# Optimization experiments

Measured on AMD Instinct MI355X. Metric: run time of the kernel, lower is better.

## Reference

```python
import jax, jax.numpy as jnp
import numpy as np

N_SAMPLES = 8_388_608   # total packed samples (~64 per ray on average)
N_RAYS = 131_072
DT_SCALE = 0.005        # keep per-ray optical depth ~O(1); also tempers global-cumsum fp32 error


def setup_inputs() -> dict:
    key = jax.random.key(0)
    k1, k2, k3, k4, k5 = jax.random.split(key, 5)
    rgb_samples = jax.random.uniform(k1, (N_SAMPLES, 3), dtype=jnp.float32)
    radiance_samples = jax.random.uniform(k2, (N_SAMPLES, 1), dtype=jnp.float32)  # density sigma >= 0
    samples_z = jax.random.uniform(k3, (N_SAMPLES,), dtype=jnp.float32)           # t values in [0,1)
    samples_dt = jax.random.uniform(k4, (N_SAMPLES,), dtype=jnp.float32) * DT_SCALE
    # sorted segment ids == contiguous packed per-ray sample ranges (ragged)
    ray_id = jnp.sort(jax.random.randint(k5, (N_SAMPLES,), 0, N_RAYS, dtype=jnp.int64))
    ray_t_exit = jnp.full((N_RAYS, 1), 2.0, dtype=jnp.float32)  # exit t beyond all z -> positive last dt
    return {
        "rgb_samples": rgb_samples,
        "radiance_samples": radiance_samples,
        "samples_z": samples_z,
        "samples_dt": samples_dt,
        "ray_id": ray_id,
        "ray_t_exit": ray_t_exit,
        "use_ray_t_exit": 1,
    }


def reference(rgb_samples, radiance_samples, samples_z, samples_dt, ray_id, ray_t_exit, use_ray_t_exit):
    N = rgb_samples.shape[0]
    sigma = radiance_samples[:, 0]
    idx = jnp.arange(N)

    # dt of the last sample of each ray is (t_exit - z_last) when use_ray_t_exit
    if use_ray_t_exit:
        last_idx = jax.ops.segment_max(idx, ray_id, num_segments=N_RAYS)
        is_last = idx == last_idx[ray_id]
        dt = jnp.where(is_last, ray_t_exit[ray_id, 0] - samples_z, samples_dt)
    else:
        dt = samples_dt

    sigdt = sigma * dt                      # optical depth per sample
    c = jnp.cumsum(sigdt)                   # global inclusive cumsum
    c_excl = c - sigdt                      # global exclusive cumsum
    # exclusive cumsum restarted per ray: subtract value at each segment's first sample
    # (c_excl is non-decreasing since sigdt >= 0, so segment_min == first element)
    seg_start = jax.ops.segment_min(c_excl, ray_id, num_segments=N_RAYS)
    T = jnp.exp(-(c_excl - seg_start[ray_id]))          # transmittance before each sample
    alpha = 1.0 - jnp.exp(-sigdt)
    w = alpha * T                                        # per-sample compositing weight

    pred_rgb = jax.ops.segment_sum(w[:, None] * rgb_samples, ray_id, num_segments=N_RAYS)   # [R,3]
    pred_depth = jax.ops.segment_sum(w * samples_z, ray_id, num_segments=N_RAYS)[:, None]   # [R,1]
    bg_transmittance = jnp.exp(-jax.ops.segment_sum(sigdt, ray_id, num_segments=N_RAYS))[:, None]  # [R,1]
    weight_per_sample = w[:, None]                                                           # [N,1]
    return pred_rgb, pred_depth, bg_transmittance, weight_per_sample
```

## Files before the change

kernel.cpp:

```cpp
#include <hip/hip_runtime.h>


#define RPW 4

struct F3 { float x, y, z; };

template <int CTRL, int ROW_MASK>
__device__ __forceinline__ float dpp_add(float x) {
    int t = __builtin_amdgcn_update_dpp(0, __float_as_int(x), CTRL, ROW_MASK, 0xf, true);
    return x + __int_as_float(t);
}

__device__ __forceinline__ float wave_incl_scan(float x) {
    x = dpp_add<0x111, 0xf>(x);
    x = dpp_add<0x112, 0xf>(x);
    x = dpp_add<0x114, 0xf>(x);
    x = dpp_add<0x118, 0xf>(x);
    x = dpp_add<0x142, 0xa>(x);
    x = dpp_add<0x143, 0xc>(x);
    return x;
}

__device__ __forceinline__ float readlane_f32(float x, int lane) {
    return __int_as_float(__builtin_amdgcn_readlane(__float_as_int(x), lane));
}

__global__ void compute_starts_kernel(const int* __restrict__ ray_id,
                                      int n_samples, int n_rays,
                                      int* __restrict__ starts) {
    const int t = blockIdx.x * blockDim.x + threadIdx.x;
    const int stride = gridDim.x * blockDim.x;
    if (t == 0) {
        const int first = ray_id[0];
        for (int r = 0; r <= first; ++r) starts[r] = 0;
        const int last = ray_id[n_samples - 1];
        for (int r = last + 1; r <= n_rays; ++r) starts[r] = n_samples;
    }
    for (int g = t; g * 4 < n_samples; g += stride) {
        const int i4 = g * 4;
        const int4 v = *reinterpret_cast<const int4*>(ray_id + i4);
        const int prev = (i4 == 0) ? v.x : ray_id[i4 - 1];
        const int vals[5] = {prev, v.x, v.y, v.z, v.w};
        #pragma unroll
        for (int j = 0; j < 4; ++j) {
            const int p = vals[j], c = vals[j + 1];
            if (c != p) {
                for (int r = p + 1; r <= c; ++r) starts[r] = i4 + j;
            }
        }
    }
}

__device__ __forceinline__ void process_chunk64(
    float sg, float zv, float dtv, F3 c,
    int base, int s1, int lane, int use_exit, float texit,
    float& csum, float& carry,
    float& accR, float& accG, float& accB, float& accD,
    float* __restrict__ out_w)
{
    const int i = base + lane;
    const bool active = i < s1;
    if (use_exit && i == s1 - 1) dtv = texit - zv;
    const float sigdt = active ? sg * dtv : 0.f;
    const float t = csum + wave_incl_scan(sigdt);
    const float v = __expf(-t);
    const int vp = __builtin_amdgcn_update_dpp(__float_as_int(carry), __float_as_int(v),
                                               0x138 , 0xf, 0xf, false);
    const float w = __int_as_float(vp) - v;
    if (active) out_w[i] = w;
    accR += w * c.x;
    accG += w * c.y;
    accB += w * c.z;
    accD += w * zv;
    csum  = readlane_f32(t, 63);
    carry = readlane_f32(v, 63);
}

__global__ __launch_bounds__(256) void render_kernel(
    const float* __restrict__ rgb,
    const float* __restrict__ sigma_in,
    const float* __restrict__ z_in,
    const float* __restrict__ dt_in,
    const float* __restrict__ t_exit,
    const int*  __restrict__ use_exit_p,
    const int*  __restrict__ starts,
    float* __restrict__ out_rgb,
    float* __restrict__ out_depth,
    float* __restrict__ out_bg,
    float* __restrict__ out_w,
    int n_rays, int n_samples)
{
    const int wave = threadIdx.x >> 6;
    const int lane = threadIdx.x & 63;
    const int wid  = blockIdx.x * (blockDim.x >> 6) + wave;
    const int ray0 = wid * RPW;
    if (ray0 >= n_rays) return;

    const int use_exit = *use_exit_p;
    const int imax = n_samples - 1;

    int s[RPW + 1];
    #pragma unroll
    for (int k = 0; k <= RPW; ++k) {
        s[k] = __builtin_amdgcn_readfirstlane(starts[min(ray0 + k, n_rays)]);
    }
    float texit[RPW];
    #pragma unroll
    for (int k = 0; k < RPW; ++k) {
        texit[k] = readlane_f32(t_exit[min(ray0 + k, n_rays - 1)], 0);
    }

    float sg1[RPW], z1[RPW], dt1[RPW];
    F3 c1[RPW];
    #pragma unroll
    for (int k = 0; k < RPW; ++k) {
        const int i1 = min(s[k] + lane, imax);
        sg1[k] = sigma_in[i1];
        z1[k]  = z_in[i1];
        dt1[k] = dt_in[i1];
        c1[k]  = *reinterpret_cast<const F3*>(rgb + 3 * (size_t)i1);
    }

    float sg2[RPW], z2[RPW], dt2[RPW];
    F3 c2[RPW];
    bool need2[RPW];
    #pragma unroll
    for (int k = 0; k < RPW; ++k) {
        need2[k] = (s[k] + 64) < s[k + 1];
        if (need2[k]) {
            const int i2 = min(s[k] + 64 + lane, imax);
            sg2[k] = sigma_in[i2];
            z2[k]  = z_in[i2];
            dt2[k] = dt_in[i2];
            c2[k]  = *reinterpret_cast<const F3*>(rgb + 3 * (size_t)i2);
        }
    }
    __builtin_amdgcn_sched_barrier(0);

    #pragma unroll
    for (int k = 0; k < RPW; ++k) {
        const int ray = ray0 + k;
        if (ray >= n_rays) break;
        const int s0 = s[k], s1 = s[k + 1];
        float csum = 0.f, carry = 1.0f;
        float accR = 0.f, accG = 0.f, accB = 0.f, accD = 0.f;

        process_chunk64(sg1[k], z1[k], dt1[k], c1[k],
                        s0, s1, lane, use_exit, texit[k],
                        csum, carry, accR, accG, accB, accD, out_w);
        if (need2[k]) {
            process_chunk64(sg2[k], z2[k], dt2[k], c2[k],
                            s0 + 64, s1, lane, use_exit, texit[k],
                            csum, carry, accR, accG, accB, accD, out_w);
        }
        for (int base = s0 + 128; base < s1; base += 64) {
            const int i = min(base + lane, imax);
            const float sg = sigma_in[i];
            const float zv = z_in[i];
            const float dtv = dt_in[i];
            const F3 cc = *reinterpret_cast<const F3*>(rgb + 3 * (size_t)i);
            process_chunk64(sg, zv, dtv, cc,
                            base, s1, lane, use_exit, texit[k],
                            csum, carry, accR, accG, accB, accD, out_w);
        }

        accR = wave_incl_scan(accR);
        accG = wave_incl_scan(accG);
        accB = wave_incl_scan(accB);
        accD = wave_incl_scan(accD);
        if (lane == 63) {
            out_rgb[3 * ray + 0] = accR;
            out_rgb[3 * ray + 1] = accG;
            out_rgb[3 * ray + 2] = accB;
            out_depth[ray] = accD;
            out_bg[ray]    = carry;
        }
    }
}

extern "C" void kernel_launch(void* const* d_in, const int* in_sizes, int n_in,
                              void* d_out, int out_size, void* d_ws, size_t ws_size,
                              hipStream_t stream) {
    const float* rgb     = (const float*)d_in[0];
    const float* sigma   = (const float*)d_in[1];
    const float* z       = (const float*)d_in[2];
    const float* dt      = (const float*)d_in[3];
    const int*   ray_id  = (const int*)d_in[4];
    const float* t_exit  = (const float*)d_in[5];
    const int*   use_ex  = (const int*)d_in[6];

    const int n_samples = in_sizes[2];
    const int n_rays    = in_sizes[5];

    int* starts = (int*)d_ws;

    float* out      = (float*)d_out;
    float* out_rgb  = out;
    float* out_dep  = out + (size_t)3 * n_rays;
    float* out_bg   = out + (size_t)4 * n_rays;
    float* out_w    = out + (size_t)5 * n_rays;

    compute_starts_kernel<<<2048, 256, 0, stream>>>(ray_id, n_samples, n_rays, starts);

    const int waves_per_block = 4;
    const int rays_per_block  = waves_per_block * RPW;
    const int blocks = (n_rays + rays_per_block - 1) / rays_per_block;
    render_kernel<<<blocks, 256, 0, stream>>>(rgb, sigma, z, dt, t_exit, use_ex,
                                              starts, out_rgb, out_dep, out_bg,
                                              out_w, n_rays, n_samples);
}
```

Baseline: 52.91 us.

## Process two samples per lane with 128-sample passes and wider loads

```diff
diff --git a/kernel.cpp b/kernel.cpp
--- a/kernel.cpp
+++ b/kernel.cpp
@@ -3,7 +3,8 @@
 
 #define RPW 4
 
-struct F3 { float x, y, z; };
+struct F2 { float x, y; };
+struct F6 { float v[6]; };
 
 template <int CTRL, int ROW_MASK>
 __device__ __forceinline__ float dpp_add(float x) {
@@ -51,29 +52,61 @@
     }
 }
 
-__device__ __forceinline__ void process_chunk64(
-    float sg, float zv, float dtv, F3 c,
-    int base, int s1, int lane, int use_exit, float texit,
+struct Slab { F2 sg, zv, dtv; F6 c; };
+
+__device__ __forceinline__ Slab load_slab(const float* __restrict__ sigma_in,
+                                          const float* __restrict__ z_in,
+                                          const float* __restrict__ dt_in,
+                                          const float* __restrict__ rgb,
+                                          int base, int lane, int n_samples)
+{
+    Slab r;
+    const int i0 = base + 2 * lane;
+    const int il = min(i0, n_samples - 2);
+    r.sg  = *reinterpret_cast<const F2*>(sigma_in + il);
+    r.zv  = *reinterpret_cast<const F2*>(z_in + il);
+    r.dtv = *reinterpret_cast<const F2*>(dt_in + il);
+    r.c   = *reinterpret_cast<const F6*>(rgb + 3 * (size_t)il);
+    if (i0 > n_samples - 2) {
+        r.sg.x = r.sg.y; r.zv.x = r.zv.y; r.dtv.x = r.dtv.y;
+        r.c.v[0] = r.c.v[3]; r.c.v[1] = r.c.v[4]; r.c.v[2] = r.c.v[5];
+    }
+    return r;
+}
+
+__device__ __forceinline__ void process_pass128(
+    const Slab& d, int base, int s1, int lane, int use_exit, float texit,
     float& csum, float& carry,
     float& accR, float& accG, float& accB, float& accD,
     float* __restrict__ out_w)
 {
-    const int i = base + lane;
-    const bool active = i < s1;
-    if (use_exit && i == s1 - 1) dtv = texit - zv;
-    const float sigdt = active ? sg * dtv : 0.f;
-    const float t = csum + wave_incl_scan(sigdt);
-    const float v = __expf(-t);
-    const int vp = __builtin_amdgcn_update_dpp(__float_as_int(carry), __float_as_int(v),
-                                               0x138 , 0xf, 0xf, false);
-    const float w = __int_as_float(vp) - v;
-    if (active) out_w[i] = w;
-    accR += w * c.x;
-    accG += w * c.y;
-    accB += w * c.z;
-    accD += w * zv;
-    csum  = readlane_f32(t, 63);
-    carry = readlane_f32(v, 63);
+    const int i0 = base + 2 * lane;
+    const int i1 = i0 + 1;
+    float dt0 = d.dtv.x, dt1v = d.dtv.y;
+    if (use_exit && i0 == s1 - 1) dt0  = texit - d.zv.x;
+    if (use_exit && i1 == s1 - 1) dt1v = texit - d.zv.y;
+    const float e0 = (i0 < s1) ? d.sg.x * dt0  : 0.f;
+    const float e1 = (i1 < s1) ? d.sg.y * dt1v : 0.f;
+
+    const float S  = wave_incl_scan(e0 + e1);
+    const float t1 = csum + S;
+    const float t0 = t1 - e1;
+    const float v0 = __expf(-t0);
+    const float v1 = __expf(-t1);
+    const int vpi = __builtin_amdgcn_update_dpp(__float_as_int(carry), __float_as_int(v1),
+                                                0x138 , 0xf, 0xf, false);
+    const float vp = __int_as_float(vpi);
+    const float w0 = vp - v0;
+    const float w1 = v0 - v1;
+
+    if (i0 < s1) out_w[i0] = w0;
+    if (i1 < s1) out_w[i1] = w1;
+    accR += w0 * d.c.v[0] + w1 * d.c.v[3];
+    accG += w0 * d.c.v[1] + w1 * d.c.v[4];
+    accB += w0 * d.c.v[2] + w1 * d.c.v[5];
+    accD += w0 * d.zv.x   + w1 * d.zv.y;
+    csum  = readlane_f32(t1, 63);
+    carry = readlane_f32(v1, 63);
 }
 
 __global__ __launch_bounds__(256) void render_kernel(
@@ -97,7 +130,6 @@
     if (ray0 >= n_rays) return;
 
     const int use_exit = *use_exit_p;
-    const int imax = n_samples - 1;
 
     int s[RPW + 1];
     #pragma unroll
@@ -110,30 +142,18 @@
         texit[k] = readlane_f32(t_exit[min(ray0 + k, n_rays - 1)], 0);
     }
 
-    float sg1[RPW], z1[RPW], dt1[RPW];
-    F3 c1[RPW];
-    #pragma unroll
-    for (int k = 0; k < RPW; ++k) {
-        const int i1 = min(s[k] + lane, imax);
-        sg1[k] = sigma_in[i1];
-        z1[k]  = z_in[i1];
-        dt1[k] = dt_in[i1];
-        c1[k]  = *reinterpret_cast<const F3*>(rgb + 3 * (size_t)i1);
-    }
-
-    float sg2[RPW], z2[RPW], dt2[RPW];
-    F3 c2[RPW];
-    bool need2[RPW];
-    #pragma unroll
-    for (int k = 0; k < RPW; ++k) {
-        need2[k] = (s[k] + 64) < s[k + 1];
-        if (need2[k]) {
-            const int i2 = min(s[k] + 64 + lane, imax);
-            sg2[k] = sigma_in[i2];
-            z2[k]  = z_in[i2];
-            dt2[k] = dt_in[i2];
-            c2[k]  = *reinterpret_cast<const F3*>(rgb + 3 * (size_t)i2);
-        }
+    Slab sl[RPW];
+    #pragma unroll
+    for (int k = 0; k < RPW; ++k) {
+        sl[k] = load_slab(sigma_in, z_in, dt_in, rgb, s[k], lane, n_samples);
+    }
+    #pragma unroll
+    for (int k = 0; k < RPW; ++k) {
+        asm volatile("" ::
+            "v"(sl[k].sg.x), "v"(sl[k].sg.y), "v"(sl[k].zv.x), "v"(sl[k].zv.y),
+            "v"(sl[k].dtv.x), "v"(sl[k].dtv.y),
+            "v"(sl[k].c.v[0]), "v"(sl[k].c.v[1]), "v"(sl[k].c.v[2]),
+            "v"(sl[k].c.v[3]), "v"(sl[k].c.v[4]), "v"(sl[k].c.v[5]));
     }
     __builtin_amdgcn_sched_barrier(0);
 
@@ -145,22 +165,12 @@
         float csum = 0.f, carry = 1.0f;
         float accR = 0.f, accG = 0.f, accB = 0.f, accD = 0.f;
 
-        process_chunk64(sg1[k], z1[k], dt1[k], c1[k],
-                        s0, s1, lane, use_exit, texit[k],
+        process_pass128(sl[k], s0, s1, lane, use_exit, texit[k],
                         csum, carry, accR, accG, accB, accD, out_w);
-        if (need2[k]) {
-            process_chunk64(sg2[k], z2[k], dt2[k], c2[k],
-                            s0 + 64, s1, lane, use_exit, texit[k],
-                            csum, carry, accR, accG, accB, accD, out_w);
-        }
-        for (int base = s0 + 128; base < s1; base += 64) {
-            const int i = min(base + lane, imax);
-            const float sg = sigma_in[i];
-            const float zv = z_in[i];
-            const float dtv = dt_in[i];
-            const F3 cc = *reinterpret_cast<const F3*>(rgb + 3 * (size_t)i);
-            process_chunk64(sg, zv, dtv, cc,
-                            base, s1, lane, use_exit, texit[k],
+
+        for (int base = s0 + 128; base < s1; base += 128) {
+            const Slab d = load_slab(sigma_in, z_in, dt_in, rgb, base, lane, n_samples);
+            process_pass128(d, base, s1, lane, use_exit, texit[k],
                             csum, carry, accR, accG, accB, accD, out_w);
         }
 
@@ -170,6 +180,7 @@
         accD = wave_incl_scan(accD);
         if (lane == 63) {
             out_rgb[3 * ray + 0] = accR;
+            out_rgb[3 * ray + 1] = accB == accB ? accG : accG;
             out_rgb[3 * ray + 1] = accG;
             out_rgb[3 * ray + 2] = accB;
             out_depth[ray] = accD;
```

After: 58.56 us. 1.11x slower.
